# Performance work log

Measured on AMD Instinct MI355X. Metric: run time of the kernel, lower is better.

Reference implementation:

```python
import jax, jax.numpy as jnp
import numpy as np

N_NODES = 100000
N_EDGES = 3200000
N_GRAPHS = 1024
F_IN = 16
H = 64
N_CLASSES = 2
EPS = 1e-5


def _seg_sum(x, ids, n):
    return jax.ops.segment_sum(x, ids, num_segments=n, indices_are_sorted=True)


def graph_norm(x, batch, weight, bias, mean_scale, n_graphs):
    # PyG GraphNorm: per-graph mean (scaled by learnable mean_scale) and variance
    cnt = jnp.maximum(_seg_sum(jnp.ones((x.shape[0], 1), x.dtype), batch, n_graphs), 1.0)
    mean = _seg_sum(x, batch, n_graphs) / cnt                      # [G, F]
    out = x - mean[batch] * mean_scale                             # [N, F]
    var = _seg_sum(out * out, batch, n_graphs) / cnt               # [G, F]
    out = out / jnp.sqrt(var + EPS)[batch]
    return weight * out + bias


def graph_conv(x, src, dst, w_rel, b_rel, w_root):
    # PyG GraphConv (aggr='add'): lin_rel(sum_{j->i} x_j) + lin_root(x_i)
    agg = jax.ops.segment_sum(x[src], dst, num_segments=x.shape[0])  # [N, F_in]
    return agg @ w_rel.T + b_rel + x @ w_root.T


def setup_inputs():
    key = jax.random.key(0)
    ks = jax.random.split(key, 32)

    def lin(k, o, i):
        return jax.random.normal(k, (o, i), jnp.float32) * (1.0 / np.sqrt(i))

    inp = {}
    inp['x'] = jax.random.normal(ks[0], (N_NODES, F_IN), jnp.float32)
    inp['edge_index'] = jax.random.randint(ks[1], (2, N_EDGES), 0, N_NODES, jnp.int32)
    inp['batch'] = jnp.sort(jax.random.randint(ks[2], (N_NODES,), 0, N_GRAPHS, jnp.int32))
    # GraphNorm params (weight, bias, mean_scale), initialized as in PyG
    for name, f in (('gn0', F_IN), ('gn1', H), ('gn2', H)):
        inp[name + '_w'] = jnp.ones((f,), jnp.float32)
        inp[name + '_b'] = jnp.zeros((f,), jnp.float32)
        inp[name + '_ms'] = jnp.ones((f,), jnp.float32)
    # GraphConv params: lin_rel (with bias) + lin_root (no bias)
    inp['w1_rel'] = lin(ks[3], H, F_IN); inp['b1'] = jnp.zeros((H,), jnp.float32); inp['w1_root'] = lin(ks[4], H, F_IN)
    inp['w2_rel'] = lin(ks[5], H, H);    inp['b2'] = jnp.zeros((H,), jnp.float32); inp['w2_root'] = lin(ks[6], H, H)
    inp['w3_rel'] = lin(ks[7], H, H);    inp['b3'] = jnp.zeros((H,), jnp.float32); inp['w3_root'] = lin(ks[8], H, H)
    inp['dense_w'] = lin(ks[9], H, H); inp['dense_b'] = jnp.zeros((H,), jnp.float32)
    inp['out_w'] = lin(ks[10], N_CLASSES, H); inp['out_b'] = jnp.zeros((N_CLASSES,), jnp.float32)
    return inp


def reference(x, edge_index, batch,
              gn0_w, gn0_b, gn0_ms, gn1_w, gn1_b, gn1_ms, gn2_w, gn2_b, gn2_ms,
              w1_rel, b1, w1_root, w2_rel, b2, w2_root, w3_rel, b3, w3_root,
              dense_w, dense_b, out_w, out_b):
    src, dst = edge_index[0], edge_index[1]
    h = graph_norm(x, batch, gn0_w, gn0_b, gn0_ms, N_GRAPHS)
    h = jax.nn.relu(graph_conv(h, src, dst, w1_rel, b1, w1_root))
    h = graph_norm(h, batch, gn1_w, gn1_b, gn1_ms, N_GRAPHS)
    h = jax.nn.relu(graph_conv(h, src, dst, w2_rel, b2, w2_root))
    h = graph_norm(h, batch, gn2_w, gn2_b, gn2_ms, N_GRAPHS)
    h = jax.nn.relu(graph_conv(h, src, dst, w3_rel, b3, w3_root))
    # global_mean_pool
    cnt = jnp.maximum(_seg_sum(jnp.ones((h.shape[0], 1), h.dtype), batch, N_GRAPHS), 1.0)
    pooled = _seg_sum(h, batch, N_GRAPHS) / cnt                    # [G, 64]
    # dropout is identity in eval mode
    g = jax.nn.relu(pooled @ dense_w.T + dense_b)
    logits = g @ out_w.T + out_b
    return jax.nn.softmax(logits, axis=1)
```

## Files before the change

kernel.cpp:

```cpp
#include <hip/hip_runtime.h>

#define NG 1024
#define GN_EPS 1e-5f
#define BSHIFT 7

typedef unsigned int u32;
typedef float f32x2 __attribute__((ext_vector_type(2)));

__device__ __forceinline__ float bflo(u32 u) {
  union { float f; u32 i; } c;
  c.i = u << 16;
  return c.f;
}
__device__ __forceinline__ float bfhi(u32 u) {
  union { float f; u32 i; } c;
  c.i = u & 0xffff0000u;
  return c.f;
}
__device__ __forceinline__ unsigned short f2bf(float f) {
  union { float f; u32 i; } c;
  c.f = f;
  u32 b = c.i;
  b += 0x7fffu + ((b >> 16) & 1u);
  return (unsigned short)(b >> 16);
}
__device__ __forceinline__ void acc8(f32x2* a, uint4 u) {
  a[0] += (f32x2){bflo(u.x), bfhi(u.x)};
  a[1] += (f32x2){bflo(u.y), bfhi(u.y)};
  a[2] += (f32x2){bflo(u.z), bfhi(u.z)};
  a[3] += (f32x2){bflo(u.w), bfhi(u.w)};
}

__global__ void k_bounds(const int* __restrict__ batch, int* __restrict__ goff, int N) {
  int i = blockIdx.x * blockDim.x + threadIdx.x;
  if (i >= N) return;
  int b = batch[i];
  int pb = (i == 0) ? -1 : batch[i - 1];
  for (int g = pb + 1; g <= b; ++g) goff[g] = i;
  if (i == N - 1) {
    for (int g = b + 1; g <= NG; ++g) goff[g] = N;
  }
}

__global__ void k_hist(const int* __restrict__ dst, int* __restrict__ bucketCnt,
                       int E, int B) {
  __shared__ int h[1024];
  for (int i = threadIdx.x; i < B; i += 256) h[i] = 0;
  __syncthreads();
  for (int e = blockIdx.x * 256 + threadIdx.x; e < E; e += gridDim.x * 256)
    atomicAdd(&h[dst[e] >> BSHIFT], 1);
  __syncthreads();
  for (int i = threadIdx.x; i < B; i += 256)
    if (h[i]) atomicAdd(&bucketCnt[i], h[i]);
}

__global__ void k_bscan(const int* __restrict__ bucketCnt, int* __restrict__ bucketOff,
                        int* __restrict__ bucketCur, int B) {
  __shared__ int lds[1024];
  int t = threadIdx.x;
  int v = (t < B) ? bucketCnt[t] : 0;
  lds[t] = v;
  __syncthreads();
  for (int off = 1; off < 1024; off <<= 1) {
    int u = (t >= off) ? lds[t - off] : 0;
    __syncthreads();
    lds[t] += u;
    __syncthreads();
  }
  if (t < B) {
    int ex = lds[t] - v;
    bucketOff[t] = ex;
    bucketCur[t] = ex;
  }
}

__global__ __launch_bounds__(256) void k_binscatter(
    const int* __restrict__ src, const int* __restrict__ dst,
    int* __restrict__ bucketCur, u32* __restrict__ ebuf,
    int E, int B, int C) {
  __shared__ int h[1024];
  __shared__ int cur[1024];
  int s = blockIdx.x * C;
  int e = min(s + C, E);
  if (s >= E) return;
  int t = threadIdx.x;
  for (int i = t; i < B; i += 256) h[i] = 0;
  __syncthreads();
  for (int k = s + t; k < e; k += 256) atomicAdd(&h[dst[k] >> BSHIFT], 1);
  __syncthreads();
  for (int i = t; i < B; i += 256) {
    int c = h[i];
    cur[i] = c ? atomicAdd(&bucketCur[i], c) : 0;
  }
  __syncthreads();
  for (int k = s + t; k < e; k += 256) {
    int d = dst[k];
    int b = d >> BSHIFT;
    int pos = atomicAdd(&cur[b], 1);
    ebuf[pos] = ((u32)(d & 127) << 24) | (u32)src[k];
  }
}

__global__ void k_bucket_fill(const u32* __restrict__ ebuf,
                              const int* __restrict__ bucketOff,
                              int* __restrict__ rowptr, int* __restrict__ col,
                              int N, int E, int B) {
  __shared__ int deg[128];
  __shared__ int cur[128];
  int b = blockIdx.x;
  int s = bucketOff[b];
  int e = (b + 1 < B) ? bucketOff[b + 1] : E;
  int t = threadIdx.x;
  int base = b << BSHIFT;
  if (t < 128) deg[t] = 0;
  __syncthreads();
  for (int k = s + t; k < e; k += 256) atomicAdd(&deg[ebuf[k] >> 24], 1);
  __syncthreads();
  if (t == 0) {
    int acc = s;
    for (int i = 0; i < 128; ++i) {
      int d = deg[i];
      deg[i] = acc;
      acc += d;
    }
  }
  __syncthreads();
  if (t < 128) {
    cur[t] = deg[t];
    int idx = base + t;
    if (idx <= N) rowptr[idx] = deg[t];
  }
  __syncthreads();
  for (int k = s + t; k < e; k += 256) {
    u32 p = ebuf[k];
    int pos = atomicAdd(&cur[p >> 24], 1);
    col[pos] = (int)(p & 0x00ffffffu);
  }
}

template <int F>
__global__ void k_gn(const float* x, float* out, unsigned short* outbf,
                     const int* __restrict__ goff,
                     const float* __restrict__ w, const float* __restrict__ b,
                     const float* __restrict__ ms) {
  constexpr int NPW = 256 / F;
  __shared__ float r1[256], r2[256];
  __shared__ float sA[F], sB[F];
  int g = blockIdx.x;
  int s = goff[g], e = goff[g + 1];
  int t = threadIdx.x;
  int f = t % F, sub = t / F;
  float s1 = 0.f, s2 = 0.f;
  for (int i = s + sub; i < e; i += NPW) {
    float v = x[i * F + f];
    s1 += v;
    s2 += v * v;
  }
  r1[t] = s1;
  r2[t] = s2;
  __syncthreads();
  if (t < F) {
    float S1 = 0.f, S2 = 0.f;
    for (int k = 0; k < NPW; ++k) {
      S1 += r1[k * F + t];
      S2 += r2[k * F + t];
    }
    float cnt = (float)max(e - s, 1);
    float mean = S1 / cnt, m2 = S2 / cnt;
    float m = ms[t];
    float var = m2 + mean * mean * m * (m - 2.f);
    float rsq = rsqrtf(var + GN_EPS);
    float Av = w[t] * rsq;
    sA[t] = Av;
    sB[t] = b[t] - mean * m * Av;
  }
  __syncthreads();
  float Af = sA[f], Bf = sB[f];
  for (int i = s + sub; i < e; i += NPW) {
    float v = x[i * F + f] * Af + Bf;
    out[i * F + f] = v;
    outbf[i * F + f] = f2bf(v);
  }
}

template <int FIN>
__global__ __launch_bounds__(256) void k_conv(
    const float* __restrict__ hin, const u32* __restrict__ hb32,
    float* __restrict__ hout,
    const int* __restrict__ rowptr, const int* __restrict__ col,
    const float* __restrict__ wrel, const float* __restrict__ brel,
    const float* __restrict__ wroot, int N) {
  constexpr int PAD = FIN + 4;
  constexpr int CPR = FIN / 2;
  constexpr int FGN = (FIN == 64) ? 8 : 2;
  constexpr int NSLOT = 64 / FGN;
  __shared__ float aggL[64 * PAD];
  int tile = blockIdx.x;
  int lane = threadIdx.x & 63;
  int w = __builtin_amdgcn_readfirstlane(threadIdx.x >> 6);

  int fg = lane & (FGN - 1);
  int slot = lane / FGN;

  for (int nl = 0; nl < 16; nl += 2) {
    int r0 = w * 16 + nl, r1 = r0 + 1;
    int n0 = tile * 64 + r0, n1 = tile * 64 + r1;
    f32x2 a0[4], b0[4], a1[4], b1[4];
#pragma unroll
    for (int j = 0; j < 4; ++j) {
      a0[j] = (f32x2){0.f, 0.f};
      b0[j] = (f32x2){0.f, 0.f};
      a1[j] = (f32x2){0.f, 0.f};
      b1[j] = (f32x2){0.f, 0.f};
    }
    int k0 = 0, e0 = 0, k1 = 0, e1 = 0;
    if (n0 < N) { k0 = rowptr[n0] + slot; e0 = rowptr[n0 + 1]; }
    if (n1 < N) { k1 = rowptr[n1] + slot; e1 = rowptr[n1 + 1]; }
    while (k0 + NSLOT < e0 && k1 + NSLOT < e1) {
      int nb00 = col[k0];
      int nb01 = col[k0 + NSLOT];
      int nb10 = col[k1];
      int nb11 = col[k1 + NSLOT];
      uint4 v00 = *(const uint4*)&hb32[(size_t)nb00 * CPR + fg * 4];
      uint4 v01 = *(const uint4*)&hb32[(size_t)nb01 * CPR + fg * 4];
      uint4 v10 = *(const uint4*)&hb32[(size_t)nb10 * CPR + fg * 4];
      uint4 v11 = *(const uint4*)&hb32[(size_t)nb11 * CPR + fg * 4];
      acc8(a0, v00);
      acc8(b0, v01);
      acc8(a1, v10);
      acc8(b1, v11);
      k0 += 2 * NSLOT;
      k1 += 2 * NSLOT;
    }
    for (; k0 + NSLOT < e0; k0 += 2 * NSLOT) {
      int nb0 = col[k0];
      int nb1 = col[k0 + NSLOT];
      uint4 v0 = *(const uint4*)&hb32[(size_t)nb0 * CPR + fg * 4];
      uint4 v1 = *(const uint4*)&hb32[(size_t)nb1 * CPR + fg * 4];
      acc8(a0, v0);
      acc8(b0, v1);
    }
    if (k0 < e0) {
      int nb = col[k0];
      uint4 v = *(const uint4*)&hb32[(size_t)nb * CPR + fg * 4];
      acc8(a0, v);
    }
    for (; k1 + NSLOT < e1; k1 += 2 * NSLOT) {
      int nb0 = col[k1];
      int nb1 = col[k1 + NSLOT];
      uint4 v0 = *(const uint4*)&hb32[(size_t)nb0 * CPR + fg * 4];
      uint4 v1 = *(const uint4*)&hb32[(size_t)nb1 * CPR + fg * 4];
      acc8(a1, v0);
      acc8(b1, v1);
    }
    if (k1 < e1) {
      int nb = col[k1];
      uint4 v = *(const uint4*)&hb32[(size_t)nb * CPR + fg * 4];
      acc8(a1, v);
    }
#pragma unroll
    for (int j = 0; j < 4; ++j) { a0[j] += b0[j]; a1[j] += b1[j]; }
#pragma unroll
    for (int m = FGN; m < 64; m <<= 1) {
#pragma unroll
      for (int j = 0; j < 4; ++j) {
        a0[j][0] += __shfl_xor(a0[j][0], m);
        a0[j][1] += __shfl_xor(a0[j][1], m);
        a1[j][0] += __shfl_xor(a1[j][0], m);
        a1[j][1] += __shfl_xor(a1[j][1], m);
      }
    }
    if (slot == 0) {
      *(float4*)&aggL[r0 * PAD + fg * 8] =
          make_float4(a0[0][0], a0[0][1], a0[1][0], a0[1][1]);
      *(float4*)&aggL[r0 * PAD + fg * 8 + 4] =
          make_float4(a0[2][0], a0[2][1], a0[3][0], a0[3][1]);
      *(float4*)&aggL[r1 * PAD + fg * 8] =
          make_float4(a1[0][0], a1[0][1], a1[1][0], a1[1][1]);
      *(float4*)&aggL[r1 * PAD + fg * 8 + 4] =
          make_float4(a1[2][0], a1[2][1], a1[3][0], a1[3][1]);
    }
  }
  __syncthreads();

  int n = tile * 64 + lane;
  if (n >= N) return;
  int wbase = w * 16;
  float accR[16], accT[16];
#pragma unroll
  for (int j = 0; j < 16; ++j) {
    accR[j] = 0.f;
    accT[j] = 0.f;
  }
#pragma unroll 2
  for (int fq = 0; fq < FIN / 4; ++fq) {
    float4 qa = *(const float4*)&aggL[lane * PAD + fq * 4];
    float4 qh = *(const float4*)&hin[(size_t)n * FIN + fq * 4];
#pragma unroll
    for (int j = 0; j < 16; ++j) {
      int o = wbase + j;
      const float* wr = &wrel[o * FIN + fq * 4];
      const float* wt = &wroot[o * FIN + fq * 4];
      accR[j] += wr[0] * qa.x + wr[1] * qa.y + wr[2] * qa.z + wr[3] * qa.w;
      accT[j] += wt[0] * qh.x + wt[1] * qh.y + wt[2] * qh.z + wt[3] * qh.w;
    }
  }
#pragma unroll
  for (int qq = 0; qq < 4; ++qq) {
    float4 rv;
    float* rr = (float*)&rv;
#pragma unroll
    for (int jj = 0; jj < 4; ++jj) {
      int j = qq * 4 + jj;
      rr[jj] = fmaxf(accR[j] + accT[j] + brel[wbase + j], 0.f);
    }
    *(float4*)&hout[(size_t)n * 64 + wbase + qq * 4] = rv;
  }
}

__global__ void k_final(const float* __restrict__ h, const int* __restrict__ goff,
                        const float* __restrict__ dw, const float* __restrict__ db,
                        const float* __restrict__ ow, const float* __restrict__ ob,
                        float* __restrict__ out) {
  __shared__ float red[256];
  __shared__ float pl[64];
  __shared__ float gl[64];
  int g = blockIdx.x;
  int s = goff[g], e = goff[g + 1];
  int t = threadIdx.x;
  int f = t & 63, sub = t >> 6;
  float s1 = 0.f;
  for (int i = s + sub; i < e; i += 4) s1 += h[i * 64 + f];
  red[t] = s1;
  __syncthreads();
  if (t < 64) {
    float S = red[t] + red[64 + t] + red[128 + t] + red[192 + t];
    float cnt = (float)max(e - s, 1);
    pl[t] = S / cnt;
  }
  __syncthreads();
  if (t < 64) {
    float acc = db[t];
#pragma unroll 8
    for (int k = 0; k < 64; ++k) acc += dw[t * 64 + k] * pl[k];
    gl[t] = fmaxf(acc, 0.f);
  }
  __syncthreads();
  if (t == 0) {
    float l0 = ob[0], l1 = ob[1];
    for (int k = 0; k < 64; ++k) {
      l0 += ow[k] * gl[k];
      l1 += ow[64 + k] * gl[k];
    }
    float m = fmaxf(l0, l1);
    float e0 = expf(l0 - m), e1 = expf(l1 - m);
    float inv = 1.f / (e0 + e1);
    out[g * 2 + 0] = e0 * inv;
    out[g * 2 + 1] = e1 * inv;
  }
}

extern "C" void kernel_launch(void* const* d_in, const int* in_sizes, int n_in,
                              void* d_out, int out_size, void* d_ws, size_t ws_size,
                              hipStream_t stream) {
  const float* x = (const float*)d_in[0];
  const int* ei = (const int*)d_in[1];
  const int* batch = (const int*)d_in[2];
  const float* gn0_w = (const float*)d_in[3];
  const float* gn0_b = (const float*)d_in[4];
  const float* gn0_ms = (const float*)d_in[5];
  const float* gn1_w = (const float*)d_in[6];
  const float* gn1_b = (const float*)d_in[7];
  const float* gn1_ms = (const float*)d_in[8];
  const float* gn2_w = (const float*)d_in[9];
  const float* gn2_b = (const float*)d_in[10];
  const float* gn2_ms = (const float*)d_in[11];
  const float* w1_rel = (const float*)d_in[12];
  const float* b1 = (const float*)d_in[13];
  const float* w1_root = (const float*)d_in[14];
  const float* w2_rel = (const float*)d_in[15];
  const float* b2 = (const float*)d_in[16];
  const float* w2_root = (const float*)d_in[17];
  const float* w3_rel = (const float*)d_in[18];
  const float* b3 = (const float*)d_in[19];
  const float* w3_root = (const float*)d_in[20];
  const float* dense_w = (const float*)d_in[21];
  const float* dense_b = (const float*)d_in[22];
  const float* out_w = (const float*)d_in[23];
  const float* out_b = (const float*)d_in[24];

  int N = in_sizes[2];
  int E = in_sizes[1] / 2;
  int B = (N >> BSHIFT) + 1;

  char* ws = (char*)d_ws;
  auto alloc = [&](size_t bytes) {
    char* p = ws;
    ws += (bytes + 255) & ~(size_t)255;
    return p;
  };
  int* rowptr = (int*)alloc(((size_t)N + 1) * 4);
  int* goff = (int*)alloc((NG + 1) * 4);
  int* bucketCnt = (int*)alloc((size_t)B * 4);
  int* bucketOff = (int*)alloc((size_t)B * 4);
  int* bucketCur = (int*)alloc((size_t)B * 4);
  int* col = (int*)alloc((size_t)E * 4);
  size_t hbytes = (size_t)N * 64 * 4;
  size_t ebytes = (size_t)E * 4;
  char* hA_raw = (char*)alloc(hbytes > ebytes ? hbytes : ebytes);
  float* hA = (float*)hA_raw;
  u32* ebuf = (u32*)hA_raw;
  float* hB = (float*)alloc(hbytes);
  unsigned short* hbf = (unsigned short*)alloc((size_t)N * 64 * 2);

  const int* src = ei;
  const int* dst = ei + E;

  hipMemsetAsync(bucketCnt, 0, (size_t)B * 4, stream);
  k_bounds<<<(N + 255) / 256, 256, 0, stream>>>(batch, goff, N);
  k_hist<<<256, 256, 0, stream>>>(dst, bucketCnt, E, B);
  k_bscan<<<1, 1024, 0, stream>>>(bucketCnt, bucketOff, bucketCur, B);
  int nbs = 192;
  int C = (E + nbs - 1) / nbs;
  k_binscatter<<<nbs, 256, 0, stream>>>(src, dst, bucketCur, ebuf, E, B, C);
  k_bucket_fill<<<B, 256, 0, stream>>>(ebuf, bucketOff, rowptr, col, N, E, B);

  int tiles = (N + 63) / 64;
  k_gn<16><<<NG, 256, 0, stream>>>(x, hA, hbf, goff, gn0_w, gn0_b, gn0_ms);
  k_conv<16><<<tiles, 256, 0, stream>>>(hA, (const u32*)hbf, hB, rowptr, col, w1_rel, b1, w1_root, N);
  k_gn<64><<<NG, 256, 0, stream>>>(hB, hB, hbf, goff, gn1_w, gn1_b, gn1_ms);
  k_conv<64><<<tiles, 256, 0, stream>>>(hB, (const u32*)hbf, hA, rowptr, col, w2_rel, b2, w2_root, N);
  k_gn<64><<<NG, 256, 0, stream>>>(hA, hA, hbf, goff, gn2_w, gn2_b, gn2_ms);
  k_conv<64><<<tiles, 256, 0, stream>>>(hA, (const u32*)hbf, hB, rowptr, col, w3_rel, b3, w3_root, N);
  k_final<<<NG, 256, 0, stream>>>(hB, goff, dense_w, dense_b, out_w, out_b, (float*)d_out);
}
```

Baseline: 506.0 us.

## Sub-sort each node's neighbors into four source-range segments for gather locality

The CSR build now splits each destination row into four sub-segments by source index range (src>>15), storing four offsets per node. The 64-feature conv kernels then process those four segments in turn, so at any moment the wavefronts tend to gather from the same ~32K-node slice of the bf16 feature table. The aim is better L2/MALL hit rates on the random gathers. In exchange there is more loop and tail overhead per row, more shared-memory histogram work in bucket_fill, and a 4x larger row-pointer array.

New measurement: 634.0 us. 1.25x slower.

```diff
diff --git a/kernel.cpp b/kernel.cpp
--- a/kernel.cpp
+++ b/kernel.cpp
@@ -103,38 +103,46 @@
 
 __global__ void k_bucket_fill(const u32* __restrict__ ebuf,
                               const int* __restrict__ bucketOff,
-                              int* __restrict__ rowptr, int* __restrict__ col,
+                              int* __restrict__ srow, int* __restrict__ col,
                               int N, int E, int B) {
-  __shared__ int deg[128];
-  __shared__ int cur[128];
+  __shared__ int deg[512];
+  __shared__ int cur[512];
   int b = blockIdx.x;
   int s = bucketOff[b];
   int e = (b + 1 < B) ? bucketOff[b + 1] : E;
   int t = threadIdx.x;
   int base = b << BSHIFT;
-  if (t < 128) deg[t] = 0;
-  __syncthreads();
-  for (int k = s + t; k < e; k += 256) atomicAdd(&deg[ebuf[k] >> 24], 1);
+  for (int i = t; i < 512; i += 256) deg[i] = 0;
+  __syncthreads();
+  for (int k = s + t; k < e; k += 256) {
+    u32 p = ebuf[k];
+    atomicAdd(&deg[(p >> 24) * 4 + ((p & 0xffffffu) >> 15)], 1);
+  }
   __syncthreads();
   if (t == 0) {
     int acc = s;
-    for (int i = 0; i < 128; ++i) {
+    for (int i = 0; i < 512; ++i) {
       int d = deg[i];
       deg[i] = acc;
       acc += d;
     }
   }
   __syncthreads();
+  for (int i = t; i < 512; i += 256) cur[i] = deg[i];
   if (t < 128) {
-    cur[t] = deg[t];
     int idx = base + t;
-    if (idx <= N) rowptr[idx] = deg[t];
-  }
+    if (idx < N) {
+#pragma unroll
+      for (int q = 0; q < 4; ++q) srow[idx * 4 + q] = deg[t * 4 + q];
+    }
+  }
+  if (b == B - 1 && t == 0) srow[4 * N] = E;
   __syncthreads();
   for (int k = s + t; k < e; k += 256) {
     u32 p = ebuf[k];
-    int pos = atomicAdd(&cur[p >> 24], 1);
-    col[pos] = (int)(p & 0x00ffffffu);
+    int sv = (int)(p & 0xffffffu);
+    int pos = atomicAdd(&cur[(p >> 24) * 4 + (sv >> 15)], 1);
+    col[pos] = sv;
   }
 }
 
@@ -187,7 +195,7 @@
 __global__ __launch_bounds__(256) void k_conv(
     const float* __restrict__ hin, const u32* __restrict__ hb32,
     float* __restrict__ hout,
-    const int* __restrict__ rowptr, const int* __restrict__ col,
+    const int* __restrict__ srow, const int* __restrict__ col,
     const float* __restrict__ wrel, const float* __restrict__ brel,
     const float* __restrict__ wroot, int N) {
   constexpr int PAD = FIN + 4;
@@ -213,51 +221,78 @@
       a1[j] = (f32x2){0.f, 0.f};
       b1[j] = (f32x2){0.f, 0.f};
     }
-    int k0 = 0, e0 = 0, k1 = 0, e1 = 0;
-    if (n0 < N) { k0 = rowptr[n0] + slot; e0 = rowptr[n0 + 1]; }
-    if (n1 < N) { k1 = rowptr[n1] + slot; e1 = rowptr[n1 + 1]; }
-    while (k0 + NSLOT < e0 && k1 + NSLOT < e1) {
-      int nb00 = col[k0];
-      int nb01 = col[k0 + NSLOT];
-      int nb10 = col[k1];
-      int nb11 = col[k1 + NSLOT];
-      uint4 v00 = *(const uint4*)&hb32[(size_t)nb00 * CPR + fg * 4];
-      uint4 v01 = *(const uint4*)&hb32[(size_t)nb01 * CPR + fg * 4];
-      uint4 v10 = *(const uint4*)&hb32[(size_t)nb10 * CPR + fg * 4];
-      uint4 v11 = *(const uint4*)&hb32[(size_t)nb11 * CPR + fg * 4];
-      acc8(a0, v00);
-      acc8(b0, v01);
-      acc8(a1, v10);
-      acc8(b1, v11);
-      k0 += 2 * NSLOT;
-      k1 += 2 * NSLOT;
-    }
-    for (; k0 + NSLOT < e0; k0 += 2 * NSLOT) {
-      int nb0 = col[k0];
-      int nb1 = col[k0 + NSLOT];
-      uint4 v0 = *(const uint4*)&hb32[(size_t)nb0 * CPR + fg * 4];
-      uint4 v1 = *(const uint4*)&hb32[(size_t)nb1 * CPR + fg * 4];
-      acc8(a0, v0);
-      acc8(b0, v1);
-    }
-    if (k0 < e0) {
-      int nb = col[k0];
-      uint4 v = *(const uint4*)&hb32[(size_t)nb * CPR + fg * 4];
-      acc8(a0, v);
-    }
-    for (; k1 + NSLOT < e1; k1 += 2 * NSLOT) {
-      int nb0 = col[k1];
-      int nb1 = col[k1 + NSLOT];
-      uint4 v0 = *(const uint4*)&hb32[(size_t)nb0 * CPR + fg * 4];
-      uint4 v1 = *(const uint4*)&hb32[(size_t)nb1 * CPR + fg * 4];
-      acc8(a1, v0);
-      acc8(b1, v1);
-    }
-    if (k1 < e1) {
-      int nb = col[k1];
-      uint4 v = *(const uint4*)&hb32[(size_t)nb * CPR + fg * 4];
-      acc8(a1, v);
-    }
+    int sr0[5], sr1[5];
+    if (n0 < N) {
+      int4 q4 = *(const int4*)&srow[4 * n0];
+      sr0[0] = q4.x; sr0[1] = q4.y; sr0[2] = q4.z; sr0[3] = q4.w;
+      sr0[4] = srow[4 * n0 + 4];
+    } else {
+#pragma unroll
+      for (int q = 0; q < 5; ++q) sr0[q] = 0;
+    }
+    if (n1 < N) {
+      int4 q4 = *(const int4*)&srow[4 * n1];
+      sr1[0] = q4.x; sr1[1] = q4.y; sr1[2] = q4.z; sr1[3] = q4.w;
+      sr1[4] = srow[4 * n1 + 4];
+    } else {
+#pragma unroll
+      for (int q = 0; q < 5; ++q) sr1[q] = 0;
+    }
+
+    auto gpair = [&](int k0, int e0, int k1, int e1) {
+      k0 += slot;
+      k1 += slot;
+      while (k0 + NSLOT < e0 && k1 + NSLOT < e1) {
+        int nb00 = col[k0];
+        int nb01 = col[k0 + NSLOT];
+        int nb10 = col[k1];
+        int nb11 = col[k1 + NSLOT];
+        uint4 v00 = *(const uint4*)&hb32[(size_t)nb00 * CPR + fg * 4];
+        uint4 v01 = *(const uint4*)&hb32[(size_t)nb01 * CPR + fg * 4];
+        uint4 v10 = *(const uint4*)&hb32[(size_t)nb10 * CPR + fg * 4];
+        uint4 v11 = *(const uint4*)&hb32[(size_t)nb11 * CPR + fg * 4];
+        acc8(a0, v00);
+        acc8(b0, v01);
+        acc8(a1, v10);
+        acc8(b1, v11);
+        k0 += 2 * NSLOT;
+        k1 += 2 * NSLOT;
+      }
+      for (; k0 + NSLOT < e0; k0 += 2 * NSLOT) {
+        int nb0 = col[k0];
+        int nb1 = col[k0 + NSLOT];
+        uint4 v0 = *(const uint4*)&hb32[(size_t)nb0 * CPR + fg * 4];
+        uint4 v1 = *(const uint4*)&hb32[(size_t)nb1 * CPR + fg * 4];
+        acc8(a0, v0);
+        acc8(b0, v1);
+      }
+      if (k0 < e0) {
+        int nb = col[k0];
+        uint4 v = *(const uint4*)&hb32[(size_t)nb * CPR + fg * 4];
+        acc8(a0, v);
+      }
+      for (; k1 + NSLOT < e1; k1 += 2 * NSLOT) {
+        int nb0 = col[k1];
+        int nb1 = col[k1 + NSLOT];
+        uint4 v0 = *(const uint4*)&hb32[(size_t)nb0 * CPR + fg * 4];
+        uint4 v1 = *(const uint4*)&hb32[(size_t)nb1 * CPR + fg * 4];
+        acc8(a1, v0);
+        acc8(b1, v1);
+      }
+      if (k1 < e1) {
+        int nb = col[k1];
+        uint4 v = *(const uint4*)&hb32[(size_t)nb * CPR + fg * 4];
+        acc8(a1, v);
+      }
+    };
+
+    if (FIN == 64) {
+#pragma unroll
+      for (int q = 0; q < 4; ++q) gpair(sr0[q], sr0[q + 1], sr1[q], sr1[q + 1]);
+    } else {
+      gpair(sr0[0], sr0[4], sr1[0], sr1[4]);
+    }
+
 #pragma unroll
     for (int j = 0; j < 4; ++j) { a0[j] += b0[j]; a1[j] += b1[j]; }
 #pragma unroll
@@ -399,7 +434,7 @@
     ws += (bytes + 255) & ~(size_t)255;
     return p;
   };
-  int* rowptr = (int*)alloc(((size_t)N + 1) * 4);
+  int* srow = (int*)alloc(((size_t)N * 4 + 1) * 4);
   int* goff = (int*)alloc((NG + 1) * 4);
   int* bucketCnt = (int*)alloc((size_t)B * 4);
   int* bucketOff = (int*)alloc((size_t)B * 4);
@@ -423,14 +458,14 @@
   int nbs = 192;
   int C = (E + nbs - 1) / nbs;
   k_binscatter<<<nbs, 256, 0, stream>>>(src, dst, bucketCur, ebuf, E, B, C);
-  k_bucket_fill<<<B, 256, 0, stream>>>(ebuf, bucketOff, rowptr, col, N, E, B);
+  k_bucket_fill<<<B, 256, 0, stream>>>(ebuf, bucketOff, srow, col, N, E, B);
 
   int tiles = (N + 63) / 64;
   k_gn<16><<<NG, 256, 0, stream>>>(x, hA, hbf, goff, gn0_w, gn0_b, gn0_ms);
-  k_conv<16><<<tiles, 256, 0, stream>>>(hA, (const u32*)hbf, hB, rowptr, col, w1_rel, b1, w1_root, N);
+  k_conv<16><<<tiles, 256, 0, stream>>>(hA, (const u32*)hbf, hB, srow, col, w1_rel, b1, w1_root, N);
   k_gn<64><<<NG, 256, 0, stream>>>(hB, hB, hbf, goff, gn1_w, gn1_b, gn1_ms);
-  k_conv<64><<<tiles, 256, 0, stream>>>(hB, (const u32*)hbf, hA, rowptr, col, w2_rel, b2, w2_root, N);
+  k_conv<64><<<tiles, 256, 0, stream>>>(hB, (const u32*)hbf, hA, srow, col, w2_rel, b2, w2_root, N);
   k_gn<64><<<NG, 256, 0, stream>>>(hA, hA, hbf, goff, gn2_w, gn2_b, gn2_ms);
-  k_conv<64><<<tiles, 256, 0, stream>>>(hA, (const u32*)hbf, hB, rowptr, col, w3_rel, b3, w3_root, N);
+  k_conv<64><<<tiles, 256, 0, stream>>>(hA, (const u32*)hbf, hB, srow, col, w3_rel, b3, w3_root, N);
   k_final<<<NG, 256, 0, stream>>>(hB, goff, dense_w, dense_b, out_w, out_b, (float*)d_out);
 }
```
